# Performance work log

Measured on AMD Instinct MI355X. Metric: run time of the kernel, lower is better.

Reference implementation:

```python
import jax, jax.numpy as jnp
from jax import lax
import numpy as np

# Straight-through sign binarization: torch code swaps .data, so autograd
# sees identity through the binarize (STE). Forward value is sign(x).
@jax.custom_vjp
def binarize(x):
    return jnp.sign(x)

def _bin_fwd(x):
    return jnp.sign(x), None

def _bin_bwd(_, g):
    return (g,)

binarize.defvjp(_bin_fwd, _bin_bwd)

EPS = 1e-5

def conv2d(x, w):
    return lax.conv_general_dilated(x, w, (1, 1), 'VALID',
                                    dimension_numbers=('NCHW', 'OIHW', 'NCHW'))

def maxpool2(x):
    return lax.reduce_window(x, -jnp.inf, lax.max, (1, 1, 2, 2), (1, 1, 2, 2), 'VALID')

def bn4(x, g, b, m, v):
    s = g / jnp.sqrt(v + EPS)
    return x * s[None, :, None, None] + (b - m * s)[None, :, None, None]

def bn2(x, g, b, m, v):
    s = g / jnp.sqrt(v + EPS)
    return x * s[None, :] + (b - m * s)[None, :]

def hardtanh(x):
    return jnp.clip(x, -1.0, 1.0)


def setup_inputs() -> dict:
    key = jax.random.key(0)
    ks = jax.random.split(key, 32)
    f32 = jnp.float32
    d = {}
    d['x'] = jax.random.normal(ks[0], (4096, 1, 32, 32), dtype=f32)
    # conv1: 1 -> 18, 5x5
    d['w1'] = jax.random.normal(ks[1], (18, 1, 5, 5), f32) * 0.1
    d['cb1'] = jax.random.normal(ks[2], (18,), f32) * 0.1
    d['g1'] = 1.0 + 0.1 * jax.random.normal(ks[3], (18,), f32)
    d['be1'] = 0.1 * jax.random.normal(ks[4], (18,), f32)
    d['m1'] = 0.1 * jax.random.normal(ks[5], (18,), f32)
    d['v1'] = 0.5 + jax.random.uniform(ks[6], (18,), f32)
    # conv2: 18 -> 48, 5x5
    d['w2'] = jax.random.normal(ks[7], (48, 18, 5, 5), f32) * 0.05
    d['cb2'] = jax.random.normal(ks[8], (48,), f32) * 0.1
    d['g2'] = 1.0 + 0.1 * jax.random.normal(ks[9], (48,), f32)
    d['be2'] = 0.1 * jax.random.normal(ks[10], (48,), f32)
    d['m2'] = 0.1 * jax.random.normal(ks[11], (48,), f32)
    d['v2'] = 0.5 + jax.random.uniform(ks[12], (48,), f32)
    # conv3: 48 -> 120, 5x5
    d['w3'] = jax.random.normal(ks[13], (120, 48, 5, 5), f32) * 0.03
    d['cb3'] = jax.random.normal(ks[14], (120,), f32) * 0.1
    d['g3'] = 1.0 + 0.1 * jax.random.normal(ks[15], (120,), f32)
    d['be3'] = 0.1 * jax.random.normal(ks[16], (120,), f32)
    d['m3'] = 0.1 * jax.random.normal(ks[17], (120,), f32)
    d['v3'] = 0.5 + jax.random.uniform(ks[18], (120,), f32)
    # fc1: 120 -> 252
    d['fw1'] = jax.random.normal(ks[19], (252, 120), f32) * 0.1
    d['fb1'] = jax.random.normal(ks[20], (252,), f32) * 0.1
    d['g4'] = 1.0 + 0.1 * jax.random.normal(ks[21], (252,), f32)
    d['be4'] = 0.1 * jax.random.normal(ks[22], (252,), f32)
    d['m4'] = 0.1 * jax.random.normal(ks[23], (252,), f32)
    d['v4'] = 0.5 + jax.random.uniform(ks[24], (252,), f32)
    # fc2: 252 -> 10
    d['fw2'] = jax.random.normal(ks[25], (10, 252), f32) * 0.1
    d['fb2'] = jax.random.normal(ks[26], (10,), f32) * 0.1
    d['g5'] = 1.0 + 0.1 * jax.random.normal(ks[27], (10,), f32)
    d['be5'] = 0.1 * jax.random.normal(ks[28], (10,), f32)
    d['m5'] = 0.1 * jax.random.normal(ks[29], (10,), f32)
    d['v5'] = 0.5 + jax.random.uniform(ks[30], (10,), f32)
    return d


def reference(x, w1, cb1, g1, be1, m1, v1,
              w2, cb2, g2, be2, m2, v2,
              w3, cb3, g3, be3, m3, v3,
              fw1, fb1, g4, be4, m4, v4,
              fw2, fb2, g5, be5, m5, v5):
    # conv1: input has 1 channel (!=3) -> binarized; weights binarized
    h = conv2d(binarize(x), binarize(w1)) + cb1[None, :, None, None]
    h = hardtanh(bn4(maxpool2(h), g1, be1, m1, v1))
    # conv2
    h = conv2d(binarize(h), binarize(w2)) + cb2[None, :, None, None]
    h = hardtanh(bn4(maxpool2(h), g2, be2, m2, v2))
    # conv3 -> [B,120,1,1]
    h = conv2d(binarize(h), binarize(w3)) + cb3[None, :, None, None]
    h = hardtanh(bn4(h, g3, be3, m3, v3))
    h = h.reshape(-1, 120)
    # fc1: input dim 120 != 784 -> binarized
    h = binarize(h) @ binarize(fw1).T + fb1[None, :]
    h = hardtanh(bn2(h, g4, be4, m4, v4))
    # fc2
    h = binarize(h) @ binarize(fw2).T + fb2[None, :]
    h = bn2(h, g5, be5, m5, v5)
    return jax.nn.log_softmax(h, axis=1)
```

## Files before the change

### kernel.cpp

```cpp
#include <hip/hip_runtime.h>
#include <stdint.h>

typedef int v4i  __attribute__((ext_vector_type(4)));
typedef int v16i __attribute__((ext_vector_type(16)));

#define W1P   0
#define INV1  18
#define CFP   20
#define THRW  104
#define INVM  152
#define B2I   160
#define W3P   12960
#define M3P   17760
#define FW1P  17880
#define M4P   18888
#define FW2P  19140

__device__ inline bool negv(int dot, float B, float S, float T) {
  float v = __fadd_rn((float)dot, B);
  v = __fmul_rn(v, S);
  v = __fadd_rn(v, T);
  return v < 0.0f;
}

__device__ inline void scanMT(float B, float S, float T, int tot, int& M, int& inv) {
  bool b0 = negv(tot, B, S, T);
  bool be = negv(-tot, B, S, T);
  if (b0 == be) { M = 0; inv = b0 ? 0 : 1; return; }
  int lo = 0, hi = tot;
  while (hi - lo > 1) {
    int mid = (lo + hi) >> 1;
    if (negv(tot - 2*mid, B, S, T) == b0) lo = mid; else hi = mid;
  }
  M = hi; inv = b0 ? 1 : 0;
}

__device__ inline float bnS(float g, float v) {
  return __fdiv_rn(g, __fsqrt_rn(__fadd_rn(v, 1e-5f)));
}
__device__ inline float bnT(float be, float m, float s) {
  return __fsub_rn(be, __fmul_rn(m, s));
}

__global__ __launch_bounds__(256) void pack_kernel(
    const float* __restrict__ w1, const float* __restrict__ w2, const float* __restrict__ w3,
    const float* __restrict__ fw1, const float* __restrict__ fw2,
    const float* __restrict__ cb1, const float* __restrict__ g1, const float* __restrict__ be1,
    const float* __restrict__ m1, const float* __restrict__ v1,
    const float* __restrict__ cb2, const float* __restrict__ g2, const float* __restrict__ be2,
    const float* __restrict__ m2, const float* __restrict__ v2,
    const float* __restrict__ cb3, const float* __restrict__ g3, const float* __restrict__ be3,
    const float* __restrict__ m3, const float* __restrict__ v3,
    const float* __restrict__ fb1, const float* __restrict__ g4, const float* __restrict__ be4,
    const float* __restrict__ m4, const float* __restrict__ v4,
    const float* __restrict__ fb2, const float* __restrict__ g5, const float* __restrict__ be5,
    const float* __restrict__ m5, const float* __restrict__ v5,
    uint32_t* __restrict__ wsu)
{
  const int tid = blockIdx.x * 256 + threadIdx.x;

  if (tid < 18) {
    int c = tid;
    uint32_t wt = 0;
    for (int ky = 0; ky < 5; ++ky)
      for (int kx = 0; kx < 5; ++kx)
        if (w1[c*25 + ky*5 + kx] < 0.0f) wt |= 1u << (ky*5 + kx);
    float S = bnS(g1[c], v1[c]);
    float B = cb1[c];
    float T = bnT(be1[c], m1[c], S);
    int M, iv; scanMT(B, S, T, 25, M, iv);
    wsu[W1P + c] = wt | ((uint32_t)M << 25);
  } else if (tid == 18) {
    uint32_t mask = 0;
    for (int c = 0; c < 18; ++c) {
      float S = bnS(g1[c], v1[c]);
      float B = cb1[c];
      float T = bnT(be1[c], m1[c], S);
      int M, iv; scanMT(B, S, T, 25, M, iv);
      if (iv) mask |= 1u << c;
    }
    wsu[INV1] = mask;
  } else if (tid >= 20 && tid < 104) {
    int j = tid - 20;
    float outv;
    if (j < 18) outv = cb1[j];
    else if (j < 36) { int c = j - 18; outv = bnS(g1[c], v1[c]); }
    else if (j < 54) { int c = j - 36; float s = bnS(g1[c], v1[c]); outv = bnT(be1[c], m1[c], s); }
    else if (j < 64) { int c = j - 54; outv = fb2[c]; }
    else if (j < 74) { int c = j - 64; outv = bnS(g5[c], v5[c]); }
    else             { int c = j - 74; float s = bnS(g5[c], v5[c]); outv = bnT(be5[c], m5[c], s); }
    wsu[CFP + j] = __float_as_uint(outv);
  } else if (tid >= 128 && tid < 192) {
    int o = tid - 128;
    bool inv = false;
    if (o < 48) {
      float S = bnS(g2[o], v2[o]);
      float B = cb2[o];
      float T = bnT(be2[o], m2[o], S);
      int M, iv; scanMT(B, S, T, 450, M, iv);
      wsu[THRW + o] = (uint32_t)(450 - 2*M);
      inv = (iv != 0);
    }
    unsigned long long bb = __ballot(inv);
    if (o == 0) {
      wsu[INVM]     = (uint32_t)bb;
      wsu[INVM + 1] = (uint32_t)(bb >> 32) & 0xFFFFu;
    }
  } else if (tid >= 256 && tid < 13056) {
    int idx = tid - 256;
    int ks   = idx >> 9;
    int slot = (idx >> 3) & 63;
    int w4   = idx & 7;
    uint32_t d = 0;
    if (slot < 48) {
      #pragma unroll
      for (int j = 0; j < 4; ++j) {
        int c = w4*4 + j;
        uint32_t byte = 0;
        if (c < 18) byte = (w2[(slot*18 + c)*25 + ks] < 0.0f) ? 0xFFu : 0x01u;
        d |= byte << (8*j);
      }
    }
    wsu[B2I + idx] = d;
  } else if (tid >= 13056 && tid < 17856) {
    int idx = tid - 13056;
    int o = idx / 40, wj = idx - o*40;
    uint32_t b = 0;
    if (wj < 25) {
      int p = wj;
      for (int c = 0; c < 32; ++c)
        if (w3[(o*48 + c)*25 + p] < 0.0f) b |= 1u << c;
    } else if (wj < 38) {
      int j = wj - 25;
      int p0 = 2*j, p1 = 2*j + 1;
      for (int q = 0; q < 16; ++q) {
        int c = 32 + q;
        if (w3[(o*48 + c)*25 + p0] < 0.0f) b |= 1u << q;
        if (p1 < 25 && w3[(o*48 + c)*25 + p1] < 0.0f) b |= 1u << (16 + q);
      }
    }
    wsu[W3P + idx] = b;
  } else if (tid >= 17856 && tid < 17976) {
    int o = tid - 17856;
    float S = bnS(g3[o], v3[o]);
    float B = cb3[o];
    float T = bnT(be3[o], m3[o], S);
    int M, iv; scanMT(B, S, T, 1200, M, iv);
    wsu[M3P + o] = (uint32_t)M | ((uint32_t)iv << 11);
  } else if (tid >= 17976 && tid < 18984) {
    int idx = tid - 17976;
    int o = idx >> 2, wi = idx & 3;
    uint32_t b = 0;
    for (int j = 0; j < 32; ++j) {
      int col = wi*32 + j;
      if (col < 120 && fw1[o*120 + col] < 0.0f) b |= 1u << j;
    }
    wsu[FW1P + idx] = b;
  } else if (tid >= 18984 && tid < 19236) {
    int o = tid - 18984;
    float S = bnS(g4[o], v4[o]);
    float B = fb1[o];
    float T = bnT(be4[o], m4[o], S);
    int M, iv; scanMT(B, S, T, 120, M, iv);
    wsu[M4P + o] = (uint32_t)M | ((uint32_t)iv << 7);
  } else if (tid >= 19236 && tid < 19316) {
    int i = tid - 19236;
    int wi = i / 10, o = i - wi*10;
    uint32_t b = 0;
    for (int j = 0; j < 32; ++j) {
      int col = wi*32 + j;
      if (col < 252 && fw2[o*252 + col] < 0.0f) b |= 1u << j;
    }
    wsu[FW2P + i] = b;
  }
}

__global__ __launch_bounds__(256, 8) void lenet_main(
    const float* __restrict__ x, const uint32_t* __restrict__ wsu,
    float* __restrict__ out)
{
  __shared__ __align__(16) uint8_t Alds[196*32];
  __shared__ uint32_t xng[32], xnz[32];
  __shared__ __align__(16) uint32_t h2p[40];
  __shared__ uint32_t h3[4];
  __shared__ uint32_t h4[8];
  __shared__ int      sthr[48];
  __shared__ uint32_t lut[16];
  __shared__ int      znz[4];

  const int t = threadIdx.x;
  const int lane = t & 63, wv = t >> 6;
  const int img = blockIdx.x;

  {
    const float* xim = x + (size_t)img * 1024;
    const int row = t >> 3, k = t & 7;
    const float4 f = ((const float4*)(xim + row*32))[k];
    const uint32_t u0 = __float_as_uint(f.x), u1 = __float_as_uint(f.y),
                   u2 = __float_as_uint(f.z), u3 = __float_as_uint(f.w);
    uint32_t ng4 = (u0>>31) | ((u1>>31)<<1) | ((u2>>31)<<2) | ((u3>>31)<<3);
    uint32_t nz4 = (uint32_t)((u0<<1)!=0u) | ((uint32_t)((u1<<1)!=0u)<<1)
                 | ((uint32_t)((u2<<1)!=0u)<<2) | ((uint32_t)((u3<<1)!=0u)<<3);
    const bool tok = (nz4 == 0xFu);
    uint32_t ng = ng4 << (4*k), nz = nz4 << (4*k);
    ng |= __shfl_xor(ng, 1);  nz |= __shfl_xor(nz, 1);
    ng |= __shfl_xor(ng, 2);  nz |= __shfl_xor(nz, 2);
    ng |= __shfl_xor(ng, 4);  nz |= __shfl_xor(nz, 4);
    if (k == 0) { xng[row] = ng; xnz[row] = nz; }
    const int wok = __all(tok);
    if (lane == 0) znz[wv] = wok;
  }

  if (t < 16) {
    uint32_t v = 0;
    #pragma unroll
    for (int b = 0; b < 4; ++b) v |= (((t >> b) & 1) ? 0xFFu : 0x01u) << (8*b);
    lut[t] = v;
  }
  if (t < 40) h2p[t] = 0;
  if (t >= 64 && t < 112) sthr[t - 64] = (int)wsu[THRW + (t - 64)];
  __syncthreads();

  const bool zer = !(znz[0] & znz[1] & znz[2] & znz[3]);
  if (t < 196) {
    const int py = t / 14, px = t - py*14;
    const int x0 = 2*px, y0 = 2*py;
    uint32_t hm = 0;
    if (!zer) {
      const uint32_t a0 = xng[y0+0] >> x0, a1 = xng[y0+1] >> x0,
                     a2 = xng[y0+2] >> x0, a3 = xng[y0+3] >> x0,
                     a4 = xng[y0+4] >> x0, a5 = xng[y0+5] >> x0;
      const uint32_t w00 = (a0&31u) | ((a1&31u)<<5) | ((a2&31u)<<10) | ((a3&31u)<<15) | ((a4&31u)<<20);
      const uint32_t w01 = ((a0>>1)&31u) | (((a1>>1)&31u)<<5) | (((a2>>1)&31u)<<10) | (((a3>>1)&31u)<<15) | (((a4>>1)&31u)<<20);
      const uint32_t w10 = (a1&31u) | ((a2&31u)<<5) | ((a3&31u)<<10) | ((a4&31u)<<15) | ((a5&31u)<<20);
      const uint32_t w11 = ((a1>>1)&31u) | (((a2>>1)&31u)<<5) | (((a3>>1)&31u)<<10) | (((a4>>1)&31u)<<15) | (((a5>>1)&31u)<<20);
      const uint32_t iv1 = wsu[INV1];
      #pragma unroll
      for (int c = 0; c < 18; ++c) {
        const uint32_t wd = wsu[W1P + c];
        const uint32_t wt = wd & 0x1FFFFFFu;
        const int M = (int)(wd >> 25);
        const int mn = min(min(__popc(w00^wt), __popc(w01^wt)),
                           min(__popc(w10^wt), __popc(w11^wt)));
        hm |= (mn >= M) ? (1u << c) : 0u;
      }
      hm ^= iv1;
    } else {
      uint32_t an[6], az[6];
      #pragma unroll
      for (int r6 = 0; r6 < 6; ++r6) { an[r6] = xng[y0+r6] >> x0; az[r6] = xnz[y0+r6] >> x0; }
      for (int c = 0; c < 18; ++c) {
        const uint32_t wt = wsu[W1P + c] & 0x1FFFFFFu;
        const float B = __uint_as_float(wsu[CFP + c]);
        const float S = __uint_as_float(wsu[CFP + 18 + c]);
        const float T = __uint_as_float(wsu[CFP + 36 + c]);
        int best = -1000;
        #pragma unroll
        for (int dy = 0; dy < 2; ++dy)
          #pragma unroll
          for (int dx = 0; dx < 2; ++dx) {
            int cnt = 0, ng = 0;
            #pragma unroll
            for (int k = 0; k < 5; ++k) {
              const uint32_t nzr = (az[dy+k] >> dx) & 31u;
              const uint32_t sgr = (an[dy+k] >> dx) & 31u;
              const uint32_t wr  = (wt >> (5*k)) & 31u;
              cnt += __popc(nzr);
              ng  += __popc((sgr ^ wr) & nzr);
            }
            const int conv = cnt - 2*ng;
            best = best > conv ? best : conv;
          }
        if (negv(best, B, S, T)) hm |= 1u << c;
      }
    }
    const uint32_t d0 = lut[hm & 15u];
    const uint32_t d1 = lut[(hm >> 4) & 15u];
    const uint32_t d2 = lut[(hm >> 8) & 15u];
    const uint32_t d3 = lut[(hm >> 12) & 15u];
    const uint32_t d4 = lut[(hm >> 16) & 15u] & 0x0000FFFFu;
    const int swz = (t & 1) << 4;
    uint8_t* ap = Alds + t*32;
    *(uint2*)(ap + swz)            = make_uint2(d0, d1);
    *(uint2*)(ap + swz + 8)        = make_uint2(d2, d3);
    *(uint2*)(ap + (swz ^ 16))     = make_uint2(d4, 0u);
    *(uint2*)(ap + (swz ^ 16) + 8) = make_uint2(0u, 0u);
  }
  __syncthreads();

  {
    const int rl = lane & 31, kh = lane >> 5;
    const int q   = (wv << 3) + (rl >> 2);
    const int qc  = q < 24 ? q : 24;
    const int wnd = rl & 3;
    const int py = qc / 5, px = qc - py*5;
    const int Y0 = 2*py + (wnd >> 1), X0 = 2*px + (wnd & 1);
    const uint32_t pbase = (uint32_t)((Y0*14 + X0) * 32);
    const uint32_t aeven = pbase + (uint32_t)(((kh ^ (X0 & 1)) & 1) << 4);
    const uint32_t aodd  = aeven ^ 16u;
    const uint8_t* bg = (const uint8_t*)(wsu + B2I) + (rl*32 + kh*16);

    v16i acc0 = {};
    v16i acc1 = {};
    #pragma unroll
    for (int ks = 0; ks < 25; ++ks) {
      const int ky = ks / 5, kx = ks - (ks/5)*5;
      const uint32_t aoff = (uint32_t)((ky*14 + kx) * 32);
      v4i a  = *(const v4i*)(Alds + ((kx & 1) ? aodd : aeven) + aoff);
      v4i b0 = *(const v4i*)(bg + ks*2048);
      v4i b1 = *(const v4i*)(bg + ks*2048 + 1024);
      acc0 = __builtin_amdgcn_mfma_i32_32x32x32_i8(a, b0, acc0, 0, 0, 0);
      acc1 = __builtin_amdgcn_mfma_i32_32x32x32_i8(a, b1, acc1, 0, 0, 0);
    }

    const int D0 = sthr[rl];
    const int D1 = sthr[rl + 32 < 47 ? rl + 32 : 47];
    const uint32_t ivm0 = wsu[INVM];
    const uint32_t ivm1d = (wsu[INVM + 1] & 0xFFFFu) * 0x10001u;
    #pragma unroll
    for (int g = 0; g < 4; ++g) {
      const int p0 = max(max(acc0[4*g], acc0[4*g+1]), max(acc0[4*g+2], acc0[4*g+3]));
      const int p1 = max(max(acc1[4*g], acc1[4*g+1]), max(acc1[4*g+2], acc1[4*g+3]));
      unsigned long long e0 = __ballot(p0 <= D0);
      unsigned long long e1 = __ballot(p1 <= D1);
      if (lane == 0) {
        const int pool = (wv << 3) + 2*g;
        if (pool < 25) {
          h2p[pool] = (uint32_t)e0 ^ ivm0;
          uint32_t hw = ((uint32_t)e1 & 0xFFFFu) | (((uint32_t)(e1 >> 32) & 0xFFFFu) << 16);
          hw ^= ivm1d;
          if (pool + 1 < 25) h2p[pool + 1] = (uint32_t)(e0 >> 32) ^ ivm0;
          else hw &= 0xFFFFu;
          h2p[25 + (pool >> 1)] = hw;
        }
      }
    }
  }
  __syncthreads();

  {
    bool pred = false;
    if (t < 240) {
      const int o = t >> 1, h = t & 1;
      const uint4* wp = (const uint4*)(wsu + W3P + o*40 + h*20);
      const uint32_t* hv = &h2p[h*20];
      int mm = 0;
      #pragma unroll
      for (int qq = 0; qq < 5; ++qq) {
        const uint4 ww = wp[qq];
        mm += __popc(hv[qq*4+0] ^ ww.x) + __popc(hv[qq*4+1] ^ ww.y)
            + __popc(hv[qq*4+2] ^ ww.z) + __popc(hv[qq*4+3] ^ ww.w);
      }
      mm += __shfl_xor(mm, 1);
      const uint32_t mw = wsu[M3P + o];
      pred = (((mm >= (int)(mw & 2047u)) ? 1u : 0u) ^ (mw >> 11)) != 0u;
    }
    unsigned long long bb = __ballot(pred && ((t & 1) == 0));
    unsigned long long xq = bb & 0x5555555555555555ull;
    xq = (xq | (xq >> 1))  & 0x3333333333333333ull;
    xq = (xq | (xq >> 2))  & 0x0F0F0F0F0F0F0F0Full;
    xq = (xq | (xq >> 4))  & 0x00FF00FF00FF00FFull;
    xq = (xq | (xq >> 8))  & 0x0000FFFF0000FFFFull;
    xq = (xq | (xq >> 16)) & 0x00000000FFFFFFFFull;
    if (lane == 0) h3[wv] = (uint32_t)xq;
  }
  __syncthreads();

  {
    bool pred = false;
    if (t < 252) {
      const uint4 fr = ((const uint4*)(wsu + FW1P))[t];
      const int mm = __popc(h3[0] ^ fr.x) + __popc(h3[1] ^ fr.y)
                   + __popc(h3[2] ^ fr.z) + __popc(h3[3] ^ fr.w);
      const uint32_t mw = wsu[M4P + t];
      pred = (((mm >= (int)(mw & 127u)) ? 1u : 0u) ^ (mw >> 7)) != 0u;
    }
    unsigned long long bb = __ballot(pred);
    if (lane == 0) {
      h4[wv*2]   = (uint32_t)bb;
      h4[wv*2+1] = (uint32_t)(bb >> 32);
    }
  }
  __syncthreads();

  if (t < 16) {
    float vv = -1e30f;
    if (t < 10) {
      int mm = 0;
      #pragma unroll
      for (int wi = 0; wi < 8; ++wi)
        mm += __popc(h4[wi] ^ wsu[FW2P + wi*10 + t]);
      const int dot = 252 - 2*mm;
      const float B = __uint_as_float(wsu[CFP + 54 + t]);
      const float S = __uint_as_float(wsu[CFP + 64 + t]);
      const float T = __uint_as_float(wsu[CFP + 74 + t]);
      float v = __fadd_rn((float)dot, B);
      v = __fmul_rn(v, S);
      vv = __fadd_rn(v, T);
    }
    float mx = vv;
    #pragma unroll
    for (int d = 1; d < 16; d <<= 1)
      mx = fmaxf(mx, __shfl_xor(mx, d, 16));
    const float sh = __fsub_rn(vv, mx);
    float s = expf(sh);
    #pragma unroll
    for (int d = 1; d < 16; d <<= 1)
      s = __fadd_rn(s, __shfl_xor(s, d, 16));
    if (t < 10)
      out[(size_t)img*10 + t] = __fsub_rn(sh, logf(s));
  }
}

extern "C" void kernel_launch(void* const* d_in, const int* in_sizes, int n_in,
                              void* d_out, int out_size, void* d_ws, size_t ws_size,
                              hipStream_t stream)
{
  const float* x   = (const float*)d_in[0];
  const float* w1  = (const float*)d_in[1];
  const float* cb1 = (const float*)d_in[2];
  const float* g1  = (const float*)d_in[3];
  const float* be1 = (const float*)d_in[4];
  const float* m1  = (const float*)d_in[5];
  const float* v1  = (const float*)d_in[6];
  const float* w2  = (const float*)d_in[7];
  const float* cb2 = (const float*)d_in[8];
  const float* g2  = (const float*)d_in[9];
  const float* be2 = (const float*)d_in[10];
  const float* m2  = (const float*)d_in[11];
  const float* v2  = (const float*)d_in[12];
  const float* w3  = (const float*)d_in[13];
  const float* cb3 = (const float*)d_in[14];
  const float* g3  = (const float*)d_in[15];
  const float* be3 = (const float*)d_in[16];
  const float* m3  = (const float*)d_in[17];
  const float* v3  = (const float*)d_in[18];
  const float* fw1 = (const float*)d_in[19];
  const float* fb1 = (const float*)d_in[20];
  const float* g4  = (const float*)d_in[21];
  const float* be4 = (const float*)d_in[22];
  const float* m4  = (const float*)d_in[23];
  const float* v4  = (const float*)d_in[24];
  const float* fw2 = (const float*)d_in[25];
  const float* fb2 = (const float*)d_in[26];
  const float* g5  = (const float*)d_in[27];
  const float* be5 = (const float*)d_in[28];
  const float* m5  = (const float*)d_in[29];
  const float* v5  = (const float*)d_in[30];

  uint32_t* wsu = (uint32_t*)d_ws;
  float* out = (float*)d_out;

  hipLaunchKernelGGL(pack_kernel, dim3(76), dim3(256), 0, stream,
                     w1, w2, w3, fw1, fw2,
                     cb1, g1, be1, m1, v1,
                     cb2, g2, be2, m2, v2,
                     cb3, g3, be3, m3, v3,
                     fb1, g4, be4, m4, v4,
                     fb2, g5, be5, m5, v5,
                     wsu);

  hipLaunchKernelGGL(lenet_main, dim3(4096), dim3(256), 0, stream,
                     x, wsu, out);
}
```

Measured before the change: 44.13 us.

## Repack conv2 K dimension as kx×channel rows to cut MFMA steps

Conv2's reduction over 18 channels × 25 taps was padded to 32 bytes per tap, which cost 25 MFMA k-steps. The new layout packs each kernel row's 5 taps × 18 channels (90 bytes, padded to 96) contiguously. The conv now takes 15 k-steps per accumulator, and the packed weights and later workspace offsets shrink to match. Conv1 outputs are gathered across 5 neighbouring pixels with shuffles to build 112-byte rows, which raises LDS use and lowers the occupancy hint to 6. The trade-off is more shuffle and packing work per thread plus possible LDS bank conflicts.

```diff
diff --git a/kernel.cpp b/kernel.cpp
--- a/kernel.cpp
+++ b/kernel.cpp
@@ -10,11 +10,11 @@
 #define THRW  104
 #define INVM  152
 #define B2I   160
-#define W3P   12960
-#define M3P   17760
-#define FW1P  17880
-#define M4P   18888
-#define FW2P  19140
+#define W3P   7840
+#define M3P   12640
+#define FW1P  12760
+#define M4P   13768
+#define FW2P  14020
 
 __device__ inline bool negv(int dot, float B, float S, float T) {
   float v = __fadd_rn((float)dot, B);
@@ -106,24 +106,28 @@
       wsu[INVM]     = (uint32_t)bb;
       wsu[INVM + 1] = (uint32_t)(bb >> 32) & 0xFFFFu;
     }
-  } else if (tid >= 256 && tid < 13056) {
+  } else if (tid >= 256 && tid < 7936) {
     int idx = tid - 256;
-    int ks   = idx >> 9;
+    int s    = idx >> 9;
     int slot = (idx >> 3) & 63;
     int w4   = idx & 7;
+    int ky = s / 3, part = s - 3*(s/3);
     uint32_t d = 0;
     if (slot < 48) {
       #pragma unroll
       for (int j = 0; j < 4; ++j) {
-        int c = w4*4 + j;
+        int g = part*32 + w4*4 + j;
         uint32_t byte = 0;
-        if (c < 18) byte = (w2[(slot*18 + c)*25 + ks] < 0.0f) ? 0xFFu : 0x01u;
+        if (g < 90) {
+          int kx = g / 18, ch = g - 18*kx;
+          byte = (w2[(slot*18 + ch)*25 + ky*5 + kx] < 0.0f) ? 0xFFu : 0x01u;
+        }
         d |= byte << (8*j);
       }
     }
     wsu[B2I + idx] = d;
-  } else if (tid >= 13056 && tid < 17856) {
-    int idx = tid - 13056;
+  } else if (tid >= 7936 && tid < 12736) {
+    int idx = tid - 7936;
     int o = idx / 40, wj = idx - o*40;
     uint32_t b = 0;
     if (wj < 25) {
@@ -140,15 +144,15 @@
       }
     }
     wsu[W3P + idx] = b;
-  } else if (tid >= 17856 && tid < 17976) {
-    int o = tid - 17856;
+  } else if (tid >= 12736 && tid < 12856) {
+    int o = tid - 12736;
     float S = bnS(g3[o], v3[o]);
     float B = cb3[o];
     float T = bnT(be3[o], m3[o], S);
     int M, iv; scanMT(B, S, T, 1200, M, iv);
     wsu[M3P + o] = (uint32_t)M | ((uint32_t)iv << 11);
-  } else if (tid >= 17976 && tid < 18984) {
-    int idx = tid - 17976;
+  } else if (tid >= 12856 && tid < 13864) {
+    int idx = tid - 12856;
     int o = idx >> 2, wi = idx & 3;
     uint32_t b = 0;
     for (int j = 0; j < 32; ++j) {
@@ -156,15 +160,15 @@
       if (col < 120 && fw1[o*120 + col] < 0.0f) b |= 1u << j;
     }
     wsu[FW1P + idx] = b;
-  } else if (tid >= 18984 && tid < 19236) {
-    int o = tid - 18984;
+  } else if (tid >= 13864 && tid < 14116) {
+    int o = tid - 13864;
     float S = bnS(g4[o], v4[o]);
     float B = fb1[o];
     float T = bnT(be4[o], m4[o], S);
     int M, iv; scanMT(B, S, T, 120, M, iv);
     wsu[M4P + o] = (uint32_t)M | ((uint32_t)iv << 7);
-  } else if (tid >= 19236 && tid < 19316) {
-    int i = tid - 19236;
+  } else if (tid >= 14116 && tid < 14196) {
+    int i = tid - 14116;
     int wi = i / 10, o = i - wi*10;
     uint32_t b = 0;
     for (int j = 0; j < 32; ++j) {
@@ -175,11 +179,11 @@
   }
 }
 
-__global__ __launch_bounds__(256, 8) void lenet_main(
+__global__ __launch_bounds__(256, 6) void lenet_main(
     const float* __restrict__ x, const uint32_t* __restrict__ wsu,
     float* __restrict__ out)
 {
-  __shared__ __align__(16) uint8_t Alds[196*32];
+  __shared__ __align__(16) uint8_t Alds[140*112];
   __shared__ uint32_t xng[32], xnz[32];
   __shared__ __align__(16) uint32_t h2p[40];
   __shared__ uint32_t h3[4];
@@ -222,69 +226,98 @@
   __syncthreads();
 
   const bool zer = !(znz[0] & znz[1] & znz[2] & znz[3]);
-  if (t < 196) {
-    const int py = t / 14, px = t - py*14;
-    const int x0 = 2*px, y0 = 2*py;
+  {
+    const int py = t >> 4, px = t & 15;
+    const bool active = (py < 14) && (px < 14);
     uint32_t hm = 0;
-    if (!zer) {
-      const uint32_t a0 = xng[y0+0] >> x0, a1 = xng[y0+1] >> x0,
-                     a2 = xng[y0+2] >> x0, a3 = xng[y0+3] >> x0,
-                     a4 = xng[y0+4] >> x0, a5 = xng[y0+5] >> x0;
-      const uint32_t w00 = (a0&31u) | ((a1&31u)<<5) | ((a2&31u)<<10) | ((a3&31u)<<15) | ((a4&31u)<<20);
-      const uint32_t w01 = ((a0>>1)&31u) | (((a1>>1)&31u)<<5) | (((a2>>1)&31u)<<10) | (((a3>>1)&31u)<<15) | (((a4>>1)&31u)<<20);
-      const uint32_t w10 = (a1&31u) | ((a2&31u)<<5) | ((a3&31u)<<10) | ((a4&31u)<<15) | ((a5&31u)<<20);
-      const uint32_t w11 = ((a1>>1)&31u) | (((a2>>1)&31u)<<5) | (((a3>>1)&31u)<<10) | (((a4>>1)&31u)<<15) | (((a5>>1)&31u)<<20);
-      const uint32_t iv1 = wsu[INV1];
+    if (active) {
+      const int x0 = 2*px, y0 = 2*py;
+      if (!zer) {
+        const uint32_t a0 = xng[y0+0] >> x0, a1 = xng[y0+1] >> x0,
+                       a2 = xng[y0+2] >> x0, a3 = xng[y0+3] >> x0,
+                       a4 = xng[y0+4] >> x0, a5 = xng[y0+5] >> x0;
+        const uint32_t w00 = (a0&31u) | ((a1&31u)<<5) | ((a2&31u)<<10) | ((a3&31u)<<15) | ((a4&31u)<<20);
+        const uint32_t w01 = ((a0>>1)&31u) | (((a1>>1)&31u)<<5) | (((a2>>1)&31u)<<10) | (((a3>>1)&31u)<<15) | (((a4>>1)&31u)<<20);
+        const uint32_t w10 = (a1&31u) | ((a2&31u)<<5) | ((a3&31u)<<10) | ((a4&31u)<<15) | ((a5&31u)<<20);
+        const uint32_t w11 = ((a1>>1)&31u) | (((a2>>1)&31u)<<5) | (((a3>>1)&31u)<<10) | (((a4>>1)&31u)<<15) | (((a5>>1)&31u)<<20);
+        const uint32_t iv1 = wsu[INV1];
+        #pragma unroll
+        for (int c = 0; c < 18; ++c) {
+          const uint32_t wd = wsu[W1P + c];
+          const uint32_t wt = wd & 0x1FFFFFFu;
+          const int M = (int)(wd >> 25);
+          const int mn = min(min(__popc(w00^wt), __popc(w01^wt)),
+                             min(__popc(w10^wt), __popc(w11^wt)));
+          hm |= (mn >= M) ? (1u << c) : 0u;
+        }
+        hm ^= iv1;
+      } else {
+        uint32_t an[6], az[6];
+        #pragma unroll
+        for (int r6 = 0; r6 < 6; ++r6) { an[r6] = xng[y0+r6] >> x0; az[r6] = xnz[y0+r6] >> x0; }
+        for (int c = 0; c < 18; ++c) {
+          const uint32_t wt = wsu[W1P + c] & 0x1FFFFFFu;
+          const float B = __uint_as_float(wsu[CFP + c]);
+          const float S = __uint_as_float(wsu[CFP + 18 + c]);
+          const float T = __uint_as_float(wsu[CFP + 36 + c]);
+          int best = -1000;
+          #pragma unroll
+          for (int dy = 0; dy < 2; ++dy)
+            #pragma unroll
+            for (int dx = 0; dx < 2; ++dx) {
+              int cnt = 0, ng = 0;
+              #pragma unroll
+              for (int k = 0; k < 5; ++k) {
+                const uint32_t nzr = (az[dy+k] >> dx) & 31u;
+                const uint32_t sgr = (an[dy+k] >> dx) & 31u;
+                const uint32_t wr  = (wt >> (5*k)) & 31u;
+                cnt += __popc(nzr);
+                ng  += __popc((sgr ^ wr) & nzr);
+              }
+              const int conv = cnt - 2*ng;
+              best = best > conv ? best : conv;
+            }
+          if (negv(best, B, S, T)) hm |= 1u << c;
+        }
+      }
+    }
+    const uint32_t m0 = hm;
+    const uint32_t m1 = __shfl_down(hm, 1);
+    const uint32_t m2 = __shfl_down(hm, 2);
+    const uint32_t m3 = __shfl_down(hm, 3);
+    const uint32_t m4 = __shfl_down(hm, 4);
+    if (py < 14 && px < 10) {
+      uint32_t e0[5], e1[5], e2[5], e3[5], e4[5];
+      const uint32_t mm[5] = {m0, m1, m2, m3, m4};
       #pragma unroll
-      for (int c = 0; c < 18; ++c) {
-        const uint32_t wd = wsu[W1P + c];
-        const uint32_t wt = wd & 0x1FFFFFFu;
-        const int M = (int)(wd >> 25);
-        const int mn = min(min(__popc(w00^wt), __popc(w01^wt)),
-                           min(__popc(w10^wt), __popc(w11^wt)));
-        hm |= (mn >= M) ? (1u << c) : 0u;
-      }
-      hm ^= iv1;
-    } else {
-      uint32_t an[6], az[6];
+      for (int k = 0; k < 5; ++k) {
+        e0[k] = lut[mm[k] & 15u];
+        e1[k] = lut[(mm[k] >> 4) & 15u];
+        e2[k] = lut[(mm[k] >> 8) & 15u];
+        e3[k] = lut[(mm[k] >> 12) & 15u];
+        e4[k] = lut[(mm[k] >> 16) & 15u] & 0xFFFFu;
+      }
+      uint32_t w[24];
+      w[0]=e0[0]; w[1]=e1[0]; w[2]=e2[0]; w[3]=e3[0];
+      w[4]  = e4[0] | (e0[1] << 16);
+      w[5]  = (e0[1] >> 16) | (e1[1] << 16);
+      w[6]  = (e1[1] >> 16) | (e2[1] << 16);
+      w[7]  = (e2[1] >> 16) | (e3[1] << 16);
+      w[8]  = (e3[1] >> 16) | (e4[1] << 16);
+      w[9]=e0[2]; w[10]=e1[2]; w[11]=e2[2]; w[12]=e3[2];
+      w[13] = e4[2] | (e0[3] << 16);
+      w[14] = (e0[3] >> 16) | (e1[3] << 16);
+      w[15] = (e1[3] >> 16) | (e2[3] << 16);
+      w[16] = (e2[3] >> 16) | (e3[3] << 16);
+      w[17] = (e3[3] >> 16) | (e4[3] << 16);
+      w[18]=e0[4]; w[19]=e1[4]; w[20]=e2[4]; w[21]=e3[4];
+      w[22] = e4[4];
+      w[23] = 0;
+      uint8_t* ap = Alds + (py*10 + px)*112;
       #pragma unroll
-      for (int r6 = 0; r6 < 6; ++r6) { an[r6] = xng[y0+r6] >> x0; az[r6] = xnz[y0+r6] >> x0; }
-      for (int c = 0; c < 18; ++c) {
-        const uint32_t wt = wsu[W1P + c] & 0x1FFFFFFu;
-        const float B = __uint_as_float(wsu[CFP + c]);
-        const float S = __uint_as_float(wsu[CFP + 18 + c]);
-        const float T = __uint_as_float(wsu[CFP + 36 + c]);
-        int best = -1000;
-        #pragma unroll
-        for (int dy = 0; dy < 2; ++dy)
-          #pragma unroll
-          for (int dx = 0; dx < 2; ++dx) {
-            int cnt = 0, ng = 0;
-            #pragma unroll
-            for (int k = 0; k < 5; ++k) {
-              const uint32_t nzr = (az[dy+k] >> dx) & 31u;
-              const uint32_t sgr = (an[dy+k] >> dx) & 31u;
-              const uint32_t wr  = (wt >> (5*k)) & 31u;
-              cnt += __popc(nzr);
-              ng  += __popc((sgr ^ wr) & nzr);
-            }
-            const int conv = cnt - 2*ng;
-            best = best > conv ? best : conv;
-          }
-        if (negv(best, B, S, T)) hm |= 1u << c;
-      }
-    }
-    const uint32_t d0 = lut[hm & 15u];
-    const uint32_t d1 = lut[(hm >> 4) & 15u];
-    const uint32_t d2 = lut[(hm >> 8) & 15u];
-    const uint32_t d3 = lut[(hm >> 12) & 15u];
-    const uint32_t d4 = lut[(hm >> 16) & 15u] & 0x0000FFFFu;
-    const int swz = (t & 1) << 4;
-    uint8_t* ap = Alds + t*32;
-    *(uint2*)(ap + swz)            = make_uint2(d0, d1);
-    *(uint2*)(ap + swz + 8)        = make_uint2(d2, d3);
-    *(uint2*)(ap + (swz ^ 16))     = make_uint2(d4, 0u);
-    *(uint2*)(ap + (swz ^ 16) + 8) = make_uint2(0u, 0u);
+      for (int q = 0; q < 6; ++q)
+        *(uint4*)(ap + q*16) = make_uint4(w[4*q], w[4*q+1], w[4*q+2], w[4*q+3]);
+    }
   }
   __syncthreads();
 
@@ -295,20 +328,17 @@
     const int wnd = rl & 3;
     const int py = qc / 5, px = qc - py*5;
     const int Y0 = 2*py + (wnd >> 1), X0 = 2*px + (wnd & 1);
-    const uint32_t pbase = (uint32_t)((Y0*14 + X0) * 32);
-    const uint32_t aeven = pbase + (uint32_t)(((kh ^ (X0 & 1)) & 1) << 4);
-    const uint32_t aodd  = aeven ^ 16u;
+    const uint8_t* abase = Alds + (Y0*10 + X0)*112 + (kh << 4);
     const uint8_t* bg = (const uint8_t*)(wsu + B2I) + (rl*32 + kh*16);
 
     v16i acc0 = {};
     v16i acc1 = {};
     #pragma unroll
-    for (int ks = 0; ks < 25; ++ks) {
-      const int ky = ks / 5, kx = ks - (ks/5)*5;
-      const uint32_t aoff = (uint32_t)((ky*14 + kx) * 32);
-      v4i a  = *(const v4i*)(Alds + ((kx & 1) ? aodd : aeven) + aoff);
-      v4i b0 = *(const v4i*)(bg + ks*2048);
-      v4i b1 = *(const v4i*)(bg + ks*2048 + 1024);
+    for (int s = 0; s < 15; ++s) {
+      const int ky = s / 3, part = s - 3*(s/3);
+      v4i a  = *(const v4i*)(abase + ky*1120 + part*32);
+      v4i b0 = *(const v4i*)(bg + s*2048);
+      v4i b1 = *(const v4i*)(bg + s*2048 + 1024);
       acc0 = __builtin_amdgcn_mfma_i32_32x32x32_i8(a, b0, acc0, 0, 0, 0);
       acc1 = __builtin_amdgcn_mfma_i32_32x32x32_i8(a, b1, acc1, 0, 0, 0);
     }
@@ -451,7 +481,7 @@
   uint32_t* wsu = (uint32_t*)d_ws;
   float* out = (float*)d_out;
 
-  hipLaunchKernelGGL(pack_kernel, dim3(76), dim3(256), 0, stream,
+  hipLaunchKernelGGL(pack_kernel, dim3(56), dim3(256), 0, stream,
                      w1, w2, w3, fw1, fw2,
                      cb1, g1, be1, m1, v1,
                      cb2, g2, be2, m2, v2,
```

Result: faster. 36.16 us (-18.0%).
